# Kernel tuning notes

Hardware: AMD Instinct MI355X
Metric: run time of the kernel (lower is better)

## Reference

```python
import jax, jax.numpy as jnp
import numpy as np

B, L, LH, D, H = 32, 512, 2048, 1024, 4
DK = D // H  # dot-attn head dim
NEG = -1e9


def _ln(x, g, b, eps=1e-5):
    m = x.mean(-1, keepdims=True)
    v = ((x - m) ** 2).mean(-1, keepdims=True)
    return (x - m) / jnp.sqrt(v + eps) * g + b


def setup_inputs() -> dict:
    key = jax.random.key(0)
    ks = jax.random.split(key, 16)
    s = 0.05
    inp = {
        "seq_emb": jax.random.normal(ks[0], (B, L, D), jnp.float32),
        "seq_mask": jnp.ones((B, L), jnp.float32),
        "his_seq_emb": jax.random.normal(ks[1], (B, LH, D), jnp.float32),
        "his_seq_mask": jnp.ones((B, LH), jnp.float32),
        # dot-product MHA (bias=True)
        "sa_wq": jax.random.normal(ks[2], (D, D), jnp.float32) * s,
        "sa_bq": jnp.zeros((D,), jnp.float32),
        "sa_wk": jax.random.normal(ks[3], (D, D), jnp.float32) * s,
        "sa_bk": jnp.zeros((D,), jnp.float32),
        "sa_wv": jax.random.normal(ks[4], (D, D), jnp.float32) * s,
        "sa_bv": jnp.zeros((D,), jnp.float32),
        "sa_wo": jax.random.normal(ks[5], (D, D), jnp.float32) * s,
        "sa_bo": jnp.zeros((D,), jnp.float32),
        # short LayerNorm
        "sn_g": jnp.ones((D,), jnp.float32),
        "sn_b": jnp.zeros((D,), jnp.float32),
        # additive MHA (h=1, bias=False)
        "aa_wq": jax.random.normal(ks[6], (D, D), jnp.float32) * s,
        "aa_wk": jax.random.normal(ks[7], (D, D), jnp.float32) * s,
        "aa_wv": jax.random.normal(ks[8], (D, D), jnp.float32) * s,
        "aa_wo": jax.random.normal(ks[9], (D, D), jnp.float32) * s,
        "aa_wa": jax.random.normal(ks[10], (D,), jnp.float32) * s,
        # long LayerNorm
        "ln_g": jnp.ones((D,), jnp.float32),
        "ln_b": jnp.zeros((D,), jnp.float32),
    }
    return inp


def reference(seq_emb, seq_mask, his_seq_emb, his_seq_mask,
              sa_wq, sa_bq, sa_wk, sa_bk, sa_wv, sa_bv, sa_wo, sa_bo,
              sn_g, sn_b, aa_wq, aa_wk, aa_wv, aa_wo, aa_wa, ln_g, ln_b):
    # ---- dot-product self attention over seq_emb (dropout = eval/no-op) ----
    def split_heads(x):  # (B,L,D) -> (B,H,L,DK)
        return x.reshape(B, -1, H, DK).transpose(0, 2, 1, 3)

    q = split_heads(seq_emb @ sa_wq + sa_bq)
    k = split_heads(seq_emb @ sa_wk + sa_bk)
    v = split_heads(seq_emb @ sa_wv + sa_bv)
    scores = jnp.einsum('bhqd,bhkd->bhqk', q, k) / jnp.sqrt(jnp.float32(DK))
    scores = jnp.where(seq_mask[:, None, None, :] == 0, NEG, scores)
    p_attn = jax.nn.softmax(scores, axis=-1)  # (B,H,L,L)
    ctx = jnp.einsum('bhqk,bhkd->bhqd', p_attn, v)
    ctx = ctx.transpose(0, 2, 1, 3).reshape(B, L, D)
    sa_out = ctx @ sa_wo + sa_bo

    poi_attn = _ln(sa_out, sn_g, sn_b) * seq_mask[:, :, None]
    poi_hidden = poi_attn.mean(axis=1, keepdims=True)  # (B,1,D)

    # ---- additive (Bahdanau) attention, h=1, Lq=1 ----
    aq = poi_hidden @ aa_wq        # (B,1,D)
    ak = his_seq_emb @ aa_wk       # (B,LH,D)
    av = his_seq_emb @ aa_wv       # (B,LH,D)
    feats = jnp.tanh(aq[:, :, None, :] + ak[:, None, :, :])  # (B,1,LH,D)
    a_scores = jnp.einsum('bqkd,d->bqk', feats, aa_wa)        # (B,1,LH)
    a_scores = jnp.where(his_seq_mask[:, None, :] == 0, NEG, a_scores)
    a_w = jax.nn.softmax(a_scores, axis=-1)
    a_ctx = jnp.einsum('bqk,bkd->bqd', a_w, av)               # (B,1,D)
    aa_out = a_ctx @ aa_wo

    his_poi_hidden = poi_hidden + _ln(aa_out, ln_g, ln_b)     # (B,1,D)

    attn_weight = p_attn[:, 0, :, :]                          # (B,L,L)
    seq_hidden = jnp.concatenate([poi_hidden, his_poi_hidden], axis=-1)[:, 0, :]  # (B,2D)
    return seq_hidden, attn_weight
```

## Files before the change

kernel.cpp:

```cpp
#include <hip/hip_runtime.h>

#define NEGV (-1000000000.0f)

typedef __attribute__((ext_vector_type(8))) short sh8;
typedef __attribute__((ext_vector_type(4))) short sh4;
typedef __attribute__((ext_vector_type(8))) __bf16 bf16x8;
typedef __attribute__((ext_vector_type(4))) float f32x4;

__device__ __forceinline__ float b2f(unsigned short u) {
  unsigned v = ((unsigned)u) << 16;
  return __builtin_bit_cast(float, v);
}
__device__ __forceinline__ unsigned short f2b(float f) {
  unsigned x = __builtin_bit_cast(unsigned, f);
  unsigned r = (x + 0x7fffu + ((x >> 16) & 1u)) >> 16;
  return (unsigned short)r;
}
__device__ __forceinline__ void g2l16(const void* g, void* l) {
  __builtin_amdgcn_global_load_lds((const __attribute__((address_space(1))) unsigned int*)g,
                                   (__attribute__((address_space(3))) unsigned int*)l, 16, 0, 0);
}
__device__ __forceinline__ f32x4 mfma16(bf16x8 a, bf16x8 b, f32x4 c) {
  return __builtin_amdgcn_mfma_f32_16x16x32_bf16(a, b, c, 0, 0, 0);
}
__device__ __forceinline__ float fast_tanh(float x) {
  x = fminf(fmaxf(x, -15.f), 15.f);
  float e = __expf(2.f * x);
  return (e - 1.f) / (e + 1.f);
}

__global__ void cvt_bf16(const float* __restrict__ src, unsigned short* __restrict__ dst, int n4) {
  int i = blockIdx.x * blockDim.x + threadIdx.x;
  int stride = gridDim.x * blockDim.x;
  for (; i < n4; i += stride) {
    float4 v = ((const float4*)src)[i];
    sh4 o;
    o[0] = (short)f2b(v.x); o[1] = (short)f2b(v.y);
    o[2] = (short)f2b(v.z); o[3] = (short)f2b(v.w);
    ((sh4*)dst)[i] = o;
  }
}

__global__ void tcvt(const float* __restrict__ src, unsigned short* __restrict__ dst) {
  __shared__ float tile[64][65];
  int bx = blockIdx.x, by = blockIdx.y;
  int tx = threadIdx.x & 63, ty = threadIdx.x >> 6;
#pragma unroll
  for (int i = 0; i < 16; ++i) {
    int r = i * 4 + ty;
    tile[r][tx] = src[(size_t)(by * 64 + r) * 1024 + bx * 64 + tx];
  }
  __syncthreads();
#pragma unroll
  for (int i = 0; i < 16; ++i) {
    int r = i * 4 + ty;
    dst[(size_t)(bx * 64 + r) * 1024 + by * 64 + tx] = f2b(tile[tx][r]);
  }
}

template<int EPI>
__global__ __launch_bounds__(512, 1)
void gemm256(const unsigned short* __restrict__ A, const unsigned short* __restrict__ Bt,
             int nbx,
             const float* __restrict__ b0, const float* __restrict__ b1,
             const float* __restrict__ b2,
             unsigned short* __restrict__ O0, unsigned short* __restrict__ O1,
             unsigned short* __restrict__ O2,
             const float* __restrict__ aq, const float* __restrict__ wa,
             float* __restrict__ sc)
{
  __shared__ char lds[131072];
  const int tid = threadIdx.x;
  const int w = tid >> 6, l = tid & 63;
  const int wm = w >> 2, wn = w & 3;
  const int lr = l & 15, g = l >> 4;
  const int swz = (lr >> 1) & 3;

  const int wg = blockIdx.x;
  const int cpx = gridDim.x >> 3;
  const int wgid = (wg & 7) * cpx + (wg >> 3);
  const int bx = wgid % nbx, by = wgid / nbx;
  const size_t m0 = (size_t)by * 256;
  const int n0 = bx * 256;

  f32x4 acc[8][4] = {};

  const int srow = tid >> 2;
  const int sk = (((tid & 3) ^ ((tid >> 3) & 3)) * 8);
  const unsigned short* gA = A + (m0 + srow) * 1024 + sk;
  const unsigned short* gB = Bt + ((size_t)n0 + srow) * 1024 + sk;
  char* const sbase = lds + w * 1024;

  const int aoff = (wm * 128 + lr) * 64 + ((g ^ swz) * 16);
  const int boff = 16384 + (wn * 64 + lr) * 64 + ((g ^ swz) * 16);

  bf16x8 af[4], bf[4], af2[4];

  auto stageA = [&](int kt) {
    const unsigned short* a = gA + kt * 32;
    char* base = sbase + ((kt & 3) << 15);
    g2l16(a, base);
    g2l16(a + 128 * 1024, base + 8192);
  };
  auto stageB = [&](int kt) {
    const unsigned short* b = gB + kt * 32;
    char* base = sbase + ((kt & 3) << 15);
    g2l16(b, base + 16384);
    g2l16(b + 128 * 1024, base + 24576);
  };
  auto loadFirst = [&](int kt) {
    const char* pb = lds + ((kt & 3) << 15);
#pragma unroll
    for (int j = 0; j < 4; ++j) bf[j] = *(const bf16x8*)(pb + boff + j * 1024);
#pragma unroll
    for (int i = 0; i < 4; ++i) af[i] = *(const bf16x8*)(pb + aoff + i * 1024);
  };

  stageA(0); stageB(0); stageA(1); stageB(1);
  asm volatile("s_waitcnt vmcnt(4)" ::: "memory");
  __builtin_amdgcn_s_barrier();
  __builtin_amdgcn_sched_barrier(0);
  loadFirst(0);
  __builtin_amdgcn_sched_barrier(0);

#pragma unroll 1
  for (int kt = 0; kt < 32; ++kt) {
    const char* pb = lds + ((kt & 3) << 15);
    if (kt < 30) stageA(kt + 2);
#pragma unroll
    for (int i = 0; i < 4; ++i) af2[i] = *(const bf16x8*)(pb + aoff + (4 + i) * 1024);
    if (kt < 30) stageB(kt + 2);
    __builtin_amdgcn_sched_barrier(0);
    __builtin_amdgcn_s_setprio(1);
#pragma unroll
    for (int i = 0; i < 4; ++i)
#pragma unroll
      for (int j = 0; j < 4; ++j)
        acc[i][j] = mfma16(af[i], bf[j], acc[i][j]);
    __builtin_amdgcn_s_setprio(0);
    __builtin_amdgcn_s_setprio(1);
#pragma unroll
    for (int i = 0; i < 4; ++i)
#pragma unroll
      for (int j = 0; j < 4; ++j)
        acc[4 + i][j] = mfma16(af2[i], bf[j], acc[4 + i][j]);
    __builtin_amdgcn_s_setprio(0);
    if (kt < 30) {
      asm volatile("s_waitcnt vmcnt(4)" ::: "memory");
    } else if (kt == 30) {
      asm volatile("s_waitcnt vmcnt(0)" ::: "memory");
    }
    __builtin_amdgcn_s_barrier();
    __builtin_amdgcn_sched_barrier(0);
    if (kt < 31) loadFirst(kt + 1);
    __builtin_amdgcn_sched_barrier(0);
  }

  if (EPI == 0) {
#pragma unroll
    for (int j = 0; j < 4; ++j) {
      int col = n0 + wn * 64 + j * 16 + lr;
      float bv = b0[col];
#pragma unroll
      for (int i = 0; i < 8; ++i) {
        size_t rowb = m0 + wm * 128 + i * 16 + g * 4;
#pragma unroll
        for (int r = 0; r < 4; ++r)
          O0[(rowb + r) * 1024 + col] = f2b(acc[i][j][r] + bv);
      }
    }
  } else if (EPI == 1) {
#pragma unroll
    for (int j = 0; j < 4; ++j) {
      int col3 = n0 + wn * 64 + j * 16 + lr;
      int part = col3 >> 10, c = col3 & 1023;
      float bv = (part == 0) ? b0[c] : (part == 1) ? b1[c] : b2[c];
      if (part < 2) {
        unsigned short* O = part == 0 ? O0 : O1;
#pragma unroll
        for (int i = 0; i < 8; ++i) {
          size_t rowb = m0 + wm * 128 + i * 16 + g * 4;
#pragma unroll
          for (int r = 0; r < 4; ++r)
            O[(rowb + r) * 1024 + c] = f2b(acc[i][j][r] + bv);
        }
      } else {
        int h = c >> 8, d = c & 255;
#pragma unroll
        for (int i = 0; i < 8; ++i) {
          size_t row = m0 + wm * 128 + i * 16 + g * 4;
          int bb = (int)(row >> 9), ll = (int)(row & 511);
          size_t base = ((size_t)(bb * 4 + h) * 256 + d) * 512 + ll;
#pragma unroll
          for (int r = 0; r < 4; ++r)
            O2[base + r] = f2b(acc[i][j][r] + bv);
        }
      }
    }
  } else {
    const int bb = (int)(m0 >> 11);
#pragma unroll
    for (int i = 0; i < 8; ++i) {
      float rp[4] = {0.f, 0.f, 0.f, 0.f};
#pragma unroll
      for (int j = 0; j < 4; ++j) {
        int col = n0 + wn * 64 + j * 16 + lr;
        float wav = wa[col];
        float aqv = aq[bb * 1024 + col];
#pragma unroll
        for (int r = 0; r < 4; ++r)
          rp[r] += wav * fast_tanh(acc[i][j][r] + aqv);
      }
#pragma unroll
      for (int off = 1; off < 16; off <<= 1)
#pragma unroll
        for (int r = 0; r < 4; ++r)
          rp[r] += __shfl_xor(rp[r], off, 64);
      if (lr == 0) {
        size_t rowb = m0 + wm * 128 + i * 16 + g * 4;
#pragma unroll
        for (int r = 0; r < 4; ++r)
          atomicAdd(&sc[rowb + r], rp[r]);
      }
    }
  }
}

__global__ __launch_bounds__(256, 4)
void attn_kernel(const unsigned short* __restrict__ q, const unsigned short* __restrict__ k,
                 const unsigned short* __restrict__ vT, const float* __restrict__ seq_mask,
                 unsigned short* __restrict__ ctx, float* __restrict__ attn_out)
{
  __shared__ char smem[34304];
  unsigned short* Qs = (unsigned short*)smem;
  unsigned short* Ps = (unsigned short*)smem;
  float* redm = (float*)(smem + 33280);
  float* reds = (float*)(smem + 33792);
  const int t = threadIdx.x, w = t >> 6, l = t & 63;
  const int lr = l & 15, g = l >> 4, lk8 = g * 8;
  const int wg = blockIdx.x;
  const int wgid = (wg & 7) * 256 + (wg >> 3);
  const int qt = wgid & 15, bh = wgid >> 4;
  const int h = bh & 3, b = bh >> 2;
  const int l0 = qt * 32;

  for (int idx = t; idx < 32 * 32; idx += 256) {
    int r = idx >> 5, ch = (idx & 31) * 8;
    *(sh8*)&Qs[r * 264 + ch] =
        *(const sh8*)&q[((size_t)(b * 512 + l0 + r)) * 1024 + h * 256 + ch];
  }
  __syncthreads();

  f32x4 accs[2][8] = {};
  const unsigned short* kbase = k + ((size_t)b * 512) * 1024 + h * 256;
#pragma unroll
  for (int ds = 0; ds < 8; ++ds) {
    int d0 = ds * 32;
    bf16x8 a0 = *(const bf16x8*)&Qs[lr * 264 + d0 + lk8];
    bf16x8 a1 = *(const bf16x8*)&Qs[(16 + lr) * 264 + d0 + lk8];
#pragma unroll
    for (int j = 0; j < 8; ++j) {
      int kj = w * 128 + j * 16 + lr;
      bf16x8 bb = *(const bf16x8*)&kbase[(size_t)kj * 1024 + d0 + lk8];
      accs[0][j] = mfma16(a0, bb, accs[0][j]);
      accs[1][j] = mfma16(a1, bb, accs[1][j]);
    }
  }

#pragma unroll
  for (int j = 0; j < 8; ++j) {
    int col = w * 128 + j * 16 + lr;
    float mv = seq_mask[b * 512 + col];
    bool msk = (mv == 0.f);
#pragma unroll
    for (int i = 0; i < 2; ++i)
#pragma unroll
      for (int r = 0; r < 4; ++r)
        accs[i][j][r] = msk ? NEGV : accs[i][j][r] * 0.0625f;
  }

  float mx[2][4], sm[2][4];
#pragma unroll
  for (int i = 0; i < 2; ++i)
#pragma unroll
    for (int r = 0; r < 4; ++r) {
      float m = accs[i][0][r];
#pragma unroll
      for (int j = 1; j < 8; ++j) m = fmaxf(m, accs[i][j][r]);
      mx[i][r] = m;
    }
#pragma unroll
  for (int off = 1; off < 16; off <<= 1)
#pragma unroll
    for (int i = 0; i < 2; ++i)
#pragma unroll
      for (int r = 0; r < 4; ++r)
        mx[i][r] = fmaxf(mx[i][r], __shfl_xor(mx[i][r], off, 64));
  if (lr == 0) {
#pragma unroll
    for (int i = 0; i < 2; ++i)
#pragma unroll
      for (int r = 0; r < 4; ++r)
        redm[w * 32 + i * 16 + g * 4 + r] = mx[i][r];
  }
  __syncthreads();
#pragma unroll
  for (int i = 0; i < 2; ++i)
#pragma unroll
    for (int r = 0; r < 4; ++r) {
      int row = i * 16 + g * 4 + r;
      mx[i][r] = fmaxf(fmaxf(redm[row], redm[32 + row]),
                       fmaxf(redm[64 + row], redm[96 + row]));
      sm[i][r] = 0.f;
    }

#pragma unroll
  for (int i = 0; i < 2; ++i)
#pragma unroll
    for (int j = 0; j < 8; ++j)
#pragma unroll
      for (int r = 0; r < 4; ++r) {
        float p = __expf(accs[i][j][r] - mx[i][r]);
        accs[i][j][r] = p;
        sm[i][r] += p;
      }
#pragma unroll
  for (int off = 1; off < 16; off <<= 1)
#pragma unroll
    for (int i = 0; i < 2; ++i)
#pragma unroll
      for (int r = 0; r < 4; ++r)
        sm[i][r] += __shfl_xor(sm[i][r], off, 64);
  if (lr == 0) {
#pragma unroll
    for (int i = 0; i < 2; ++i)
#pragma unroll
      for (int r = 0; r < 4; ++r)
        reds[w * 32 + i * 16 + g * 4 + r] = sm[i][r];
  }
  __syncthreads();
#pragma unroll
  for (int i = 0; i < 2; ++i)
#pragma unroll
    for (int r = 0; r < 4; ++r) {
      int row = i * 16 + g * 4 + r;
      float s = reds[row] + reds[32 + row] + reds[64 + row] + reds[96 + row];
      sm[i][r] = 1.f / s;
    }

#pragma unroll
  for (int i = 0; i < 2; ++i)
#pragma unroll
    for (int j = 0; j < 8; ++j) {
      int col = w * 128 + j * 16 + lr;
#pragma unroll
      for (int r = 0; r < 4; ++r) {
        int row = i * 16 + g * 4 + r;
        float pn = accs[i][j][r] * sm[i][r];
        Ps[row * 520 + col] = f2b(pn);
        if (h == 0)
          attn_out[((size_t)(b * 512 + l0 + row)) * 512 + col] = pn;
      }
    }
  __syncthreads();

  f32x4 acco[2][4] = {};
  const unsigned short* vbase = vT + ((size_t)(b * 4 + h)) * 256 * 512;
#pragma unroll
  for (int ks = 0; ks < 16; ++ks) {
    int kj0 = ks * 32;
    bf16x8 a0 = *(const bf16x8*)&Ps[lr * 520 + kj0 + lk8];
    bf16x8 a1 = *(const bf16x8*)&Ps[(16 + lr) * 520 + kj0 + lk8];
#pragma unroll
    for (int j = 0; j < 4; ++j) {
      int d = w * 64 + j * 16 + lr;
      bf16x8 bb = *(const bf16x8*)&vbase[(size_t)d * 512 + kj0 + lk8];
      acco[0][j] = mfma16(a0, bb, acco[0][j]);
      acco[1][j] = mfma16(a1, bb, acco[1][j]);
    }
  }
#pragma unroll
  for (int i = 0; i < 2; ++i)
#pragma unroll
    for (int j = 0; j < 4; ++j) {
      int col = w * 64 + j * 16 + lr;
#pragma unroll
      for (int r = 0; r < 4; ++r) {
        int row = i * 16 + g * 4 + r;
        ctx[((size_t)(b * 512 + l0 + row)) * 1024 + h * 256 + col] = f2b(acco[i][j][r]);
      }
    }
}

__global__ __launch_bounds__(256)
void ln_mean(const unsigned short* __restrict__ sa, const float* __restrict__ g,
             const float* __restrict__ bt, const float* __restrict__ mask,
             float* __restrict__ poi_sum)
{
  const int b = blockIdx.y, ch = blockIdx.x;
  const int t = threadIdx.x, w = t >> 6, l = t & 63;
  float gg[16], bb[16];
#pragma unroll
  for (int j = 0; j < 16; ++j) { gg[j] = g[l * 16 + j]; bb[j] = bt[l * 16 + j]; }
  float accv[16];
#pragma unroll
  for (int j = 0; j < 16; ++j) accv[j] = 0.f;
  for (int rr = 0; rr < 16; ++rr) {
    int row = ch * 64 + w * 16 + rr;
    const unsigned short* rp = sa + ((size_t)(b * 512 + row)) * 1024 + l * 16;
    float x[16];
    sh8 v0 = *(const sh8*)rp;
    sh8 v1 = *(const sh8*)(rp + 8);
#pragma unroll
    for (int j = 0; j < 8; ++j) {
      x[j] = b2f((unsigned short)v0[j]);
      x[8 + j] = b2f((unsigned short)v1[j]);
    }
    float s = 0.f, s2 = 0.f;
#pragma unroll
    for (int j = 0; j < 16; ++j) { s += x[j]; s2 += x[j] * x[j]; }
#pragma unroll
    for (int off = 1; off < 64; off <<= 1) {
      s += __shfl_xor(s, off, 64);
      s2 += __shfl_xor(s2, off, 64);
    }
    float mean = s * (1.f / 1024.f);
    float var = s2 * (1.f / 1024.f) - mean * mean;
    float rinv = rsqrtf(var + 1e-5f);
    float mk = mask[b * 512 + row];
#pragma unroll
    for (int j = 0; j < 16; ++j) accv[j] += ((x[j] - mean) * rinv * gg[j] + bb[j]) * mk;
  }
#pragma unroll
  for (int j = 0; j < 16; ++j) atomicAdd(&poi_sum[b * 1024 + l * 16 + j], accv[j]);
}

__global__ void finalize_poi(const float* __restrict__ ps, float* __restrict__ poi) {
  int i = blockIdx.x * 256 + threadIdx.x;
  if (i < 32 * 1024) poi[i] = ps[i] * (1.f / 512.f);
}

__global__ __launch_bounds__(256)
void gemv32(const float* __restrict__ in, const float* __restrict__ W, float* __restrict__ out)
{
  const int b = blockIdx.y;
  const int n = blockIdx.x * 256 + threadIdx.x;
  const float* ib = in + b * 1024;
  float acc = 0.f;
  for (int d = 0; d < 1024; d += 4) {
    acc += ib[d]     * W[(size_t)d * 1024 + n]
         + ib[d + 1] * W[(size_t)(d + 1) * 1024 + n]
         + ib[d + 2] * W[(size_t)(d + 2) * 1024 + n]
         + ib[d + 3] * W[(size_t)(d + 3) * 1024 + n];
  }
  out[b * 1024 + n] = acc;
}

__global__ __launch_bounds__(256)
void softmax_his(float* __restrict__ sc, const float* __restrict__ mask)
{
  __shared__ float red[4];
  const int b = blockIdx.x, t = threadIdx.x, w = t >> 6, l = t & 63;
  float v[8];
  float mx = -3.0e38f;
#pragma unroll
  for (int i = 0; i < 8; ++i) {
    int kk = t + i * 256;
    float s = (mask[b * 2048 + kk] == 0.f) ? NEGV : sc[b * 2048 + kk];
    v[i] = s;
    mx = fmaxf(mx, s);
  }
#pragma unroll
  for (int off = 1; off < 64; off <<= 1) mx = fmaxf(mx, __shfl_xor(mx, off, 64));
  if (l == 0) red[w] = mx;
  __syncthreads();
  mx = fmaxf(fmaxf(red[0], red[1]), fmaxf(red[2], red[3]));
  float sum = 0.f;
#pragma unroll
  for (int i = 0; i < 8; ++i) { v[i] = __expf(v[i] - mx); sum += v[i]; }
#pragma unroll
  for (int off = 1; off < 64; off <<= 1) sum += __shfl_xor(sum, off, 64);
  __syncthreads();
  if (l == 0) red[w] = sum;
  __syncthreads();
  sum = red[0] + red[1] + red[2] + red[3];
  float inv = 1.f / sum;
#pragma unroll
  for (int i = 0; i < 8; ++i) sc[b * 2048 + t + i * 256] = v[i] * inv;
}

__global__ __launch_bounds__(256)
void hw_kernel(const float* __restrict__ aw, const unsigned short* __restrict__ his,
               float* __restrict__ hw)
{
  const int b = blockIdx.y, kc = blockIdx.x, t = threadIdx.x;
  const int cb = t * 4;
  float a0 = 0.f, a1 = 0.f, a2 = 0.f, a3 = 0.f;
  for (int kk = 0; kk < 256; ++kk) {
    int k = kc * 256 + kk;
    float wg = aw[b * 2048 + k];
    sh4 vv = *(const sh4*)&his[((size_t)(b * 2048 + k)) * 1024 + cb];
    a0 += wg * b2f((unsigned short)vv[0]);
    a1 += wg * b2f((unsigned short)vv[1]);
    a2 += wg * b2f((unsigned short)vv[2]);
    a3 += wg * b2f((unsigned short)vv[3]);
  }
  atomicAdd(&hw[b * 1024 + cb + 0], a0);
  atomicAdd(&hw[b * 1024 + cb + 1], a1);
  atomicAdd(&hw[b * 1024 + cb + 2], a2);
  atomicAdd(&hw[b * 1024 + cb + 3], a3);
}

__global__ __launch_bounds__(256)
void final_kernel(const float* __restrict__ aa_out, const float* __restrict__ g,
                  const float* __restrict__ bt, const float* __restrict__ poi,
                  float* __restrict__ out)
{
  __shared__ float r1[4], r2[4];
  const int b = blockIdx.x, t = threadIdx.x, w = t >> 6, l = t & 63;
  float x[4];
#pragma unroll
  for (int j = 0; j < 4; ++j) x[j] = aa_out[b * 1024 + t * 4 + j];
  float s = 0.f, s2 = 0.f;
#pragma unroll
  for (int j = 0; j < 4; ++j) { s += x[j]; s2 += x[j] * x[j]; }
#pragma unroll
  for (int off = 1; off < 64; off <<= 1) {
    s += __shfl_xor(s, off, 64);
    s2 += __shfl_xor(s2, off, 64);
  }
  if (l == 0) { r1[w] = s; r2[w] = s2; }
  __syncthreads();
  s = r1[0] + r1[1] + r1[2] + r1[3];
  s2 = r2[0] + r2[1] + r2[2] + r2[3];
  float mean = s * (1.f / 1024.f);
  float var = s2 * (1.f / 1024.f) - mean * mean;
  float rinv = rsqrtf(var + 1e-5f);
#pragma unroll
  for (int j = 0; j < 4; ++j) {
    int c = t * 4 + j;
    float lnv = (x[j] - mean) * rinv * g[c] + bt[c];
    float pv = poi[b * 1024 + c];
    out[b * 2048 + c] = pv;
    out[b * 2048 + 1024 + c] = pv + lnv;
  }
}

extern "C" void kernel_launch(void* const* d_in, const int* in_sizes, int n_in,
                              void* d_out, int out_size, void* d_ws, size_t ws_size,
                              hipStream_t stream)
{
  const float* seq_emb  = (const float*)d_in[0];
  const float* seq_mask = (const float*)d_in[1];
  const float* his_emb  = (const float*)d_in[2];
  const float* his_mask = (const float*)d_in[3];
  const float* sa_wq = (const float*)d_in[4];
  const float* sa_bq = (const float*)d_in[5];
  const float* sa_wk = (const float*)d_in[6];
  const float* sa_bk = (const float*)d_in[7];
  const float* sa_wv = (const float*)d_in[8];
  const float* sa_bv = (const float*)d_in[9];
  const float* sa_wo = (const float*)d_in[10];
  const float* sa_bo = (const float*)d_in[11];
  const float* sn_g  = (const float*)d_in[12];
  const float* sn_b  = (const float*)d_in[13];
  const float* aa_wq = (const float*)d_in[14];
  const float* aa_wk = (const float*)d_in[15];
  const float* aa_wv = (const float*)d_in[16];
  const float* aa_wo = (const float*)d_in[17];
  const float* aa_wa = (const float*)d_in[18];
  const float* ln_g  = (const float*)d_in[19];
  const float* ln_b  = (const float*)d_in[20];
  float* out = (float*)d_out;

  char* p = (char*)d_ws;
  size_t off = 0;
  auto alloc = [&](size_t bytes) -> void* {
    void* r = p + off;
    off += (bytes + 255) & ~(size_t)255;
    return r;
  };
  unsigned short* seqb = (unsigned short*)alloc((size_t)16384 * 1024 * 2);
  unsigned short* hisb = (unsigned short*)alloc((size_t)65536 * 1024 * 2);
  unsigned short* wcat = (unsigned short*)alloc((size_t)3072 * 1024 * 2);
  unsigned short* woT  = (unsigned short*)alloc((size_t)1024 * 1024 * 2);
  unsigned short* awkT = (unsigned short*)alloc((size_t)1024 * 1024 * 2);
  unsigned short* qb   = (unsigned short*)alloc((size_t)16384 * 1024 * 2);
  unsigned short* kb   = (unsigned short*)alloc((size_t)16384 * 1024 * 2);
  unsigned short* vTb  = (unsigned short*)alloc((size_t)16384 * 1024 * 2);
  unsigned short* ctxb = (unsigned short*)alloc((size_t)16384 * 1024 * 2);
  unsigned short* saob = (unsigned short*)alloc((size_t)16384 * 1024 * 2);
  float* poi_sum = (float*)alloc((size_t)32 * 1024 * 4);
  float* poi     = (float*)alloc((size_t)32 * 1024 * 4);
  float* aqb     = (float*)alloc((size_t)32 * 1024 * 4);
  float* ascore  = (float*)alloc((size_t)32 * 2048 * 4);
  float* hwb     = (float*)alloc((size_t)32 * 1024 * 4);
  float* actx    = (float*)alloc((size_t)32 * 1024 * 4);
  float* aaout   = (float*)alloc((size_t)32 * 1024 * 4);
  if (off > ws_size) return;

  hipMemsetAsync(poi_sum, 0, (size_t)32 * 1024 * 4, stream);
  hipMemsetAsync(ascore, 0, (size_t)32 * 2048 * 4, stream);
  hipMemsetAsync(hwb, 0, (size_t)32 * 1024 * 4, stream);

  cvt_bf16<<<2048, 256, 0, stream>>>(seq_emb, seqb, 16384 * 1024 / 4);
  cvt_bf16<<<2048, 256, 0, stream>>>(his_emb, hisb, 65536 * 1024 / 4);
  dim3 tg(16, 16);
  tcvt<<<tg, 256, 0, stream>>>(sa_wq, wcat);
  tcvt<<<tg, 256, 0, stream>>>(sa_wk, wcat + (size_t)1024 * 1024);
  tcvt<<<tg, 256, 0, stream>>>(sa_wv, wcat + (size_t)2048 * 1024);
  tcvt<<<tg, 256, 0, stream>>>(sa_wo, woT);
  tcvt<<<tg, 256, 0, stream>>>(aa_wk, awkT);

  gemm256<1><<<768, 512, 0, stream>>>(seqb, wcat, 12, sa_bq, sa_bk, sa_bv,
                                      qb, kb, vTb, nullptr, nullptr, nullptr);

  attn_kernel<<<2048, 256, 0, stream>>>(qb, kb, vTb, seq_mask, ctxb, out + 65536);

  gemm256<0><<<256, 512, 0, stream>>>(ctxb, woT, 4, sa_bo, nullptr, nullptr,
                                      saob, nullptr, nullptr, nullptr, nullptr, nullptr);
  ln_mean<<<dim3(8, 32), 256, 0, stream>>>(saob, sn_g, sn_b, seq_mask, poi_sum);
  finalize_poi<<<128, 256, 0, stream>>>(poi_sum, poi);
  gemv32<<<dim3(4, 32), 256, 0, stream>>>(poi, aa_wq, aqb);

  gemm256<2><<<1024, 512, 0, stream>>>(hisb, awkT, 4, nullptr, nullptr, nullptr,
                                       nullptr, nullptr, nullptr, aqb, aa_wa, ascore);
  softmax_his<<<32, 256, 0, stream>>>(ascore, his_mask);
  hw_kernel<<<dim3(8, 32), 256, 0, stream>>>(ascore, hisb, hwb);
  gemv32<<<dim3(4, 32), 256, 0, stream>>>(hwb, aa_wv, actx);
  gemv32<<<dim3(4, 32), 256, 0, stream>>>(actx, aa_wo, aaout);
  final_kernel<<<32, 256, 0, stream>>>(aaout, ln_g, ln_b, poi, out);
}
```

Measured before the change: 795.6 us.

## Deepen GEMM pipeline to three stages with register double-buffered fragments

Restructures the projection GEMM main loop to prefetch three K-tiles into LDS instead of two. It also double-buffers the full A/B register fragments so the LDS reads for the next tile are issued before the current tile's MFMAs. The loop is manually unrolled by two to alternate register buffers. This targets LDS-read and global-load latency that was previously exposed between MFMA groups, at the cost of roughly doubling fragment register usage, which may reduce occupancy or cause spills.

Measured after the change: 802.6 us. No clear change (+0.9%).

```diff
diff --git a/kernel.cpp b/kernel.cpp
--- a/kernel.cpp
+++ b/kernel.cpp
@@ -84,6 +84,7 @@
   const int n0 = bx * 256;
 
   f32x4 acc[8][4] = {};
+  bf16x8 fa[2][8], fb[2][4];
 
   const int srow = tid >> 2;
   const int sk = (((tid & 3) ^ ((tid >> 3) & 3)) * 8);
@@ -94,67 +95,64 @@
   const int aoff = (wm * 128 + lr) * 64 + ((g ^ swz) * 16);
   const int boff = 16384 + (wn * 64 + lr) * 64 + ((g ^ swz) * 16);
 
-  bf16x8 af[4], bf[4], af2[4];
-
-  auto stageA = [&](int kt) {
+  auto stageAB = [&](int kt) {
     const unsigned short* a = gA + kt * 32;
+    const unsigned short* b = gB + kt * 32;
     char* base = sbase + ((kt & 3) << 15);
     g2l16(a, base);
     g2l16(a + 128 * 1024, base + 8192);
-  };
-  auto stageB = [&](int kt) {
-    const unsigned short* b = gB + kt * 32;
-    char* base = sbase + ((kt & 3) << 15);
     g2l16(b, base + 16384);
     g2l16(b + 128 * 1024, base + 24576);
   };
-  auto loadFirst = [&](int kt) {
-    const char* pb = lds + ((kt & 3) << 15);
-#pragma unroll
-    for (int j = 0; j < 4; ++j) bf[j] = *(const bf16x8*)(pb + boff + j * 1024);
-#pragma unroll
-    for (int i = 0; i < 4; ++i) af[i] = *(const bf16x8*)(pb + aoff + i * 1024);
-  };
-
-  stageA(0); stageB(0); stageA(1); stageB(1);
+
+  stageAB(0); stageAB(1); stageAB(2);
   asm volatile("s_waitcnt vmcnt(4)" ::: "memory");
   __builtin_amdgcn_s_barrier();
+  {
+    const char* p0 = lds;
+#pragma unroll
+    for (int j = 0; j < 4; ++j) fb[0][j] = *(const bf16x8*)(p0 + boff + j * 1024);
+#pragma unroll
+    for (int i = 0; i < 8; ++i) fa[0][i] = *(const bf16x8*)(p0 + aoff + i * 1024);
+  }
   __builtin_amdgcn_sched_barrier(0);
-  loadFirst(0);
-  __builtin_amdgcn_sched_barrier(0);
+
+#define GITER(KTV, CUR, NXT)                                                   \
+  {                                                                            \
+    const int kt_ = (KTV);                                                     \
+    if (kt_ < 29) stageAB(kt_ + 3);                                            \
+    if (kt_ < 31) {                                                            \
+      const char* pn_ = lds + (((kt_ + 1) & 3) << 15);                         \
+      _Pragma("unroll")                                                        \
+      for (int j = 0; j < 4; ++j)                                              \
+        fb[NXT][j] = *(const bf16x8*)(pn_ + boff + j * 1024);                  \
+      _Pragma("unroll")                                                        \
+      for (int i = 0; i < 8; ++i)                                              \
+        fa[NXT][i] = *(const bf16x8*)(pn_ + aoff + i * 1024);                  \
+    }                                                                          \
+    __builtin_amdgcn_sched_barrier(0);                                         \
+    __builtin_amdgcn_s_setprio(1);                                             \
+    _Pragma("unroll")                                                          \
+    for (int i = 0; i < 8; ++i)                                                \
+      _Pragma("unroll")                                                        \
+      for (int j = 0; j < 4; ++j)                                              \
+        acc[i][j] = mfma16(fa[CUR][i], fb[CUR][j], acc[i][j]);                 \
+    __builtin_amdgcn_s_setprio(0);                                             \
+    if (kt_ < 29) { asm volatile("s_waitcnt vmcnt(4)" ::: "memory"); }         \
+    else if (kt_ == 29) { asm volatile("s_waitcnt vmcnt(0)" ::: "memory"); }   \
+    if (kt_ < 31) __builtin_amdgcn_s_barrier();                                \
+  }
 
 #pragma unroll 1
-  for (int kt = 0; kt < 32; ++kt) {
-    const char* pb = lds + ((kt & 3) << 15);
-    if (kt < 30) stageA(kt + 2);
-#pragma unroll
-    for (int i = 0; i < 4; ++i) af2[i] = *(const bf16x8*)(pb + aoff + (4 + i) * 1024);
-    if (kt < 30) stageB(kt + 2);
-    __builtin_amdgcn_sched_barrier(0);
-    __builtin_amdgcn_s_setprio(1);
-#pragma unroll
-    for (int i = 0; i < 4; ++i)
-#pragma unroll
-      for (int j = 0; j < 4; ++j)
-        acc[i][j] = mfma16(af[i], bf[j], acc[i][j]);
-    __builtin_amdgcn_s_setprio(0);
-    __builtin_amdgcn_s_setprio(1);
-#pragma unroll
-    for (int i = 0; i < 4; ++i)
-#pragma unroll
-      for (int j = 0; j < 4; ++j)
-        acc[4 + i][j] = mfma16(af2[i], bf[j], acc[4 + i][j]);
-    __builtin_amdgcn_s_setprio(0);
-    if (kt < 30) {
-      asm volatile("s_waitcnt vmcnt(4)" ::: "memory");
-    } else if (kt == 30) {
-      asm volatile("s_waitcnt vmcnt(0)" ::: "memory");
-    }
-    __builtin_amdgcn_s_barrier();
-    __builtin_amdgcn_sched_barrier(0);
-    if (kt < 31) loadFirst(kt + 1);
-    __builtin_amdgcn_sched_barrier(0);
-  }
+  for (int kk = 0; kk < 28; kk += 2) {
+    GITER(kk, 0, 1)
+    GITER(kk + 1, 1, 0)
+  }
+  GITER(28, 0, 1)
+  GITER(29, 1, 0)
+  GITER(30, 0, 1)
+  GITER(31, 1, 0)
+#undef GITER
 
   if (EPI == 0) {
 #pragma unroll
```
